# Kernel optimization log

Hardware: AMD Instinct MI355X
Metric: run time of the kernel (lower is better)

## Reference

```python
import jax
import jax.numpy as jnp
from jax import lax
import numpy as np

BETA = 0.5
IPOT_ITERS = 50
IPOT_K = 1
EPS = 1e-5  # F.normalize eps


def _l2_normalize(x, eps=EPS):
    n = jnp.linalg.norm(x, axis=-1, keepdims=True)
    return x / jnp.maximum(n, eps)


def cost_matrix_cosine(x, y):
    # x: [b, m, d], y: [b, n, d] -> 1 - cosine_sim : [b, m, n]
    return 1.0 - jnp.einsum('bmd,bnd->bmn', _l2_normalize(x), _l2_normalize(y))


def ipot(C, x_len, x_pad, y_len, y_pad, joint_pad, beta, iteration, k):
    # C: [b, m, n] (txt x img). Mirrors UNITER's ipot (no_grad).
    b, m, n = C.shape
    jp_T = jnp.swapaxes(joint_pad, 1, 2)                      # [b, n, m]
    A = jnp.where(jp_T, 0.0, jnp.exp(-jnp.swapaxes(C, 1, 2) / beta))  # [b, n, m]
    T0 = jnp.where(jp_T, 0.0, jnp.ones((b, n, m), C.dtype))
    sigma0 = jnp.where(x_pad, 0.0, 1.0 / x_len[:, None])      # [b, m]
    xl = x_len[:, None, None]
    yl = y_len[:, None, None]
    x_mask = (x_pad.astype(C.dtype) * 1e4)[:, None, :]        # [b, 1, m]
    y_mask = (y_pad.astype(C.dtype) * 1e4)[:, None, :]        # [b, 1, n]

    def outer(carry, _):
        T, sigma = carry
        Q = A * T                                             # [b, n, m]
        def inner(sig, _):
            # sig: [b, m]
            qs = jnp.einsum('bnm,bm->bn', Q, sig)[:, None, :]  # [b, 1, n]
            delta = 1.0 / (yl * qs + y_mask)                   # [b, 1, n]
            sig_new = 1.0 / (xl * jnp.matmul(delta, Q) + x_mask)  # [b, 1, m]
            return sig_new[:, 0, :], delta
        sigma, deltas = lax.scan(inner, sigma, None, length=k)
        delta = deltas[-1]                                     # [b, 1, n]
        T = delta[:, 0, :, None] * Q * sigma[:, None, :]       # [b, n, m]
        return (T, sigma), None

    (T, _), _ = lax.scan(outer, (T0, sigma0), None, length=iteration)
    return jnp.where(jp_T, 0.0, T)


def optimal_transport_dist(txt_emb, img_emb, txt_pad, img_pad,
                           beta=BETA, iteration=IPOT_ITERS, k=IPOT_K):
    cost = cost_matrix_cosine(txt_emb, img_emb)               # [b, tl, il]
    joint_pad = txt_pad[:, :, None] | img_pad[:, None, :]
    cost = jnp.where(joint_pad, 0.0, cost)
    txt_len = (txt_pad.shape[1] - jnp.sum(txt_pad, axis=1)).astype(cost.dtype)
    img_len = (img_pad.shape[1] - jnp.sum(img_pad, axis=1)).astype(cost.dtype)
    T = ipot(lax.stop_gradient(cost), txt_len, txt_pad, img_len, img_pad,
             joint_pad, beta, iteration, k)                   # [b, il, tl]
    T = lax.stop_gradient(T)
    # trace(cost @ T) without materializing [b, tl, tl]
    return jnp.einsum('bmn,bnm->b', cost, T)


def setup_inputs() -> dict:
    key = jax.random.key(0)
    ks = jax.random.split(key, 6)
    B, TL, IL, D = 256, 128, 100, 768
    sequence_output = jax.random.normal(ks[0], (B, TL + IL, D), dtype=jnp.float32)
    input_ids = jax.random.randint(ks[1], (B, TL), 0, 30522)
    image_feat = jax.random.normal(ks[2], (B, IL, D), dtype=jnp.float32)
    # realistic padding: valid prefix of random length, padded suffix
    txt_len = jax.random.randint(ks[3], (B,), TL // 2, TL + 1)
    img_len = jax.random.randint(ks[4], (B,), IL // 2, IL + 1)
    txt_pad = jnp.arange(TL)[None, :] >= txt_len[:, None]
    img_pad = jnp.arange(IL)[None, :] >= img_len[:, None]
    is_correct = jax.random.randint(ks[5], (B,), 0, 2)
    return {
        'sequence_output': sequence_output,
        'input_ids': input_ids,
        'image_feat': image_feat,
        'txt_pad': txt_pad,
        'img_pad': img_pad,
        'is_correct': is_correct,
    }


def reference(sequence_output, input_ids, image_feat, txt_pad, img_pad, is_correct):
    tl = input_ids.shape[1]
    il = image_feat.shape[1]
    txt_emb = sequence_output[:, :tl, :].astype(jnp.float32)
    img_emb = sequence_output[:, tl:tl + il, :].astype(jnp.float32)
    ot_dist = optimal_transport_dist(txt_emb, img_emb, txt_pad, img_pad)
    ot_dist = ot_dist.astype(sequence_output.dtype)
    pos = is_correct == 1
    neg = is_correct == 0
    pos_sum = jnp.sum(jnp.where(pos, ot_dist, 0.0))
    neg_sum = jnp.sum(jnp.where(neg, ot_dist, 0.0))
    denom = jnp.sum(pos) + jnp.sum(neg)
    ot_loss = (pos_sum - neg_sum) / denom.astype(ot_dist.dtype)
    return ot_loss


if __name__ == '__main__':
    out = reference(**setup_inputs())
    print(out)
```

## Files before the change

### kernel.cpp

```cpp
#include <hip/hip_runtime.h>
#include <math.h>
#include <stdint.h>

#define TL 128
#define IL 100
#define NP 112
#define DIM 768
#define NSEQ 228
#define KT 32
#define NT 512
#define NWAVE 8
#define ITERS 50
#define XROW 72

typedef float f32x4 __attribute__((ext_vector_type(4)));
typedef short short8 __attribute__((ext_vector_type(8)));

__device__ __forceinline__ uint16_t f2bf(float x) {
    union { float f; uint32_t u; } v; v.f = x;
    uint32_t r = v.u + 0x7FFFu + ((v.u >> 16) & 1u);
    return (uint16_t)(r >> 16);
}
__device__ __forceinline__ float bf2f(uint16_t h) {
    union { float f; uint32_t u; } v; v.u = ((uint32_t)h) << 16;
    return v.f;
}

__device__ __forceinline__ float xorsum32(float x) {
    x += __shfl_xor(x, 1);
    x += __shfl_xor(x, 2);
    x += __shfl_xor(x, 4);
    x += __shfl_xor(x, 8);
    x += __shfl_xor(x, 16);
    return x;
}

__global__ void __launch_bounds__(NT, 2)
WRA_ot_kernel(const float* __restrict__ seq,
              const int* __restrict__ txt_pad,
              const int* __restrict__ img_pad,
              const int* __restrict__ is_correct,
              float* __restrict__ out, int nblocks)
{
    __shared__ __align__(16) union {
        struct {
            uint16_t X[TL * XROW];
            uint16_t Y[NP * XROW];
        } g;
        float As[448 * 32];
        float wp[2][7][TL];
    } u;
    __shared__ __align__(16) float sums[NSEQ];
    __shared__ __align__(16) float xm[TL];
    __shared__ __align__(16) float ym[NP];
    __shared__ __align__(16) float inx[TL];
    __shared__ __align__(16) float iny[NP];
    __shared__ float red[NWAVE];
    __shared__ int cnt[2];

    const int t    = threadIdx.x;
    const int b    = blockIdx.x;
    const int w    = t >> 6;
    const int lane = t & 63;

    if (t < 2) cnt[t] = 0;
    if (t < NSEQ) sums[t] = 0.0f;
    __syncthreads();
    if (t < TL) {
        int p = txt_pad[b * TL + t] ? 1 : 0;
        xm[t] = p ? 1e4f : 0.0f;
        if (p) atomicAdd(&cnt[0], 1);
    } else if (t < TL + IL) {
        int p = img_pad[b * IL + (t - TL)] ? 1 : 0;
        ym[t - TL] = p ? 1e4f : 0.0f;
        if (p) atomicAdd(&cnt[1], 1);
    } else if (t < TL + NP) {
        ym[t - TL] = 1e4f;
    }

    const float* Xg = seq + (size_t)b * NSEQ * DIM;
    const float* Yg = Xg + (size_t)TL * DIM;

    const float* gp[4];
    uint16_t*    dp[4];
    int   srow[4];
    bool  act[4];
    float nrm[4];
    float4 v[4];
#pragma unroll
    for (int r = 0; r < 4; r++) {
        int f = t + NT * r;
        act[r] = (f < 1824);
        nrm[r] = 0.0f;
        int f2 = act[r] ? f : 0;
        bool isX = (f2 < 1024);
        int row = isX ? (f2 >> 3) : ((f2 - 1024) >> 3);
        int kc  = (f2 & 7) << 2;
        gp[r] = (isX ? Xg : Yg) + row * DIM + kc;
        int nq  = ((kc >> 3) + row) & 3;
        dp[r] = (isX ? u.g.X : u.g.Y) + row * XROW + nq * 8 + (kc & 7);
        srow[r] = isX ? row : (TL + row);
    }
    {
        uint32_t* y32 = (uint32_t*)u.g.Y;
        for (int i = IL * (XROW/2) + t; i < NP * (XROW/2); i += NT) y32[i] = 0;
    }
#pragma unroll
    for (int r = 0; r < 4; r++) if (act[r]) v[r] = *(const float4*)(gp[r]);

    const int wm = w >> 1;
    const int wn = w & 1;
    const int NQ = wn ? 3 : 4;
    f32x4 acc[2][4];
#pragma unroll
    for (int a = 0; a < 2; a++)
#pragma unroll
        for (int q = 0; q < 4; q++) acc[a][q] = (f32x4){0.f, 0.f, 0.f, 0.f};

    const int lr = lane & 15, lq = lane >> 4;
    for (int c = 0; c < 24; c++) {
        __syncthreads();
#pragma unroll
        for (int r = 0; r < 4; r++) if (act[r]) {
            float4 x = v[r];
            nrm[r] += x.x*x.x + x.y*x.y + x.z*x.z + x.w*x.w;
            uint16_t h0 = f2bf(x.x), h1 = f2bf(x.y), h2 = f2bf(x.z), h3 = f2bf(x.w);
            uint16_t l0 = f2bf(x.x - bf2f(h0)), l1 = f2bf(x.y - bf2f(h1));
            uint16_t l2 = f2bf(x.z - bf2f(h2)), l3 = f2bf(x.w - bf2f(h3));
            uint64_t hq  = (uint64_t)h0 | ((uint64_t)h1<<16) | ((uint64_t)h2<<32) | ((uint64_t)h3<<48);
            uint64_t lq8 = (uint64_t)l0 | ((uint64_t)l1<<16) | ((uint64_t)l2<<32) | ((uint64_t)l3<<48);
            *(uint64_t*)(dp[r])      = hq;
            *(uint64_t*)(dp[r] + 32) = lq8;
            if (c < 23) v[r] = *(const float4*)(gp[r] + (c + 1) * KT);
        }
        __syncthreads();
        short8 ah[2], al[2], bh[4], bl[4];
#pragma unroll
        for (int a = 0; a < 2; a++) {
            int m = 16 * (2*wm + a) + lr;
            int base = m * XROW + 8 * ((lq + m) & 3);
            ah[a] = *(const short8*)&u.g.X[base];
            al[a] = *(const short8*)&u.g.X[base + 32];
        }
#pragma unroll
        for (int q = 0; q < 4; q++) if (q < NQ) {
            int n = 16 * (4*wn + q) + lr;
            int base = n * XROW + 8 * ((lq + n) & 3);
            bh[q] = *(const short8*)&u.g.Y[base];
            bl[q] = *(const short8*)&u.g.Y[base + 32];
        }
#pragma unroll
        for (int a = 0; a < 2; a++)
#pragma unroll
            for (int q = 0; q < 4; q++) if (q < NQ) {
                acc[a][q] = __builtin_amdgcn_mfma_f32_16x16x32_bf16(ah[a], bh[q], acc[a][q], 0, 0, 0);
                acc[a][q] = __builtin_amdgcn_mfma_f32_16x16x32_bf16(ah[a], bl[q], acc[a][q], 0, 0, 0);
                acc[a][q] = __builtin_amdgcn_mfma_f32_16x16x32_bf16(al[a], bh[q], acc[a][q], 0, 0, 0);
            }
    }

    __syncthreads();
#pragma unroll
    for (int r = 0; r < 4; r++) if (act[r]) atomicAdd(&sums[srow[r]], nrm[r]);
#pragma unroll
    for (int a = 0; a < 2; a++)
#pragma unroll
        for (int q = 0; q < 4; q++) if (q < NQ)
#pragma unroll
            for (int rg = 0; rg < 4; rg++) {
                int m = 16 * (2*wm + a) + 4*lq + rg;
                int n = 16 * (4*wn + q) + lr;
                int tp = (m >> 2) + ((n >> 3) << 5);
                int cell = (((n & 7) ^ (tp & 7)) << 2) + (m & 3);
                u.As[(tp << 5) + cell] = acc[a][q][rg];
            }
    __syncthreads();
    if (t < TL)            inx[t]      = 1.0f / fmaxf(sqrtf(sums[t]), 1e-5f);
    else if (t < NSEQ)     iny[t - TL] = 1.0f / fmaxf(sqrtf(sums[t]), 1e-5f);
    else if (t < TL + NP)  iny[t - TL] = 1.0f;
    __syncthreads();

    const float xlen = (float)(TL - cnt[0]);
    const float ylen = (float)(IL - cnt[1]);
    const int mI = lane & 31;
    const int nI = t >> 5;
    const bool activeN = (nI < 14);

    float rx[4], xmv[4], ry[8], ymv[8];
    {
        float4 a0 = *(const float4*)&inx[4*mI];
        rx[0]=a0.x; rx[1]=a0.y; rx[2]=a0.z; rx[3]=a0.w;
        float4 b0 = *(const float4*)&xm[4*mI];
        xmv[0]=b0.x; xmv[1]=b0.y; xmv[2]=b0.z; xmv[3]=b0.w;
        if (activeN) {
            float4 c0 = *(const float4*)&iny[8*nI], c1 = *(const float4*)&iny[8*nI + 4];
            ry[0]=c0.x; ry[1]=c0.y; ry[2]=c0.z; ry[3]=c0.w;
            ry[4]=c1.x; ry[5]=c1.y; ry[6]=c1.z; ry[7]=c1.w;
            float4 d0 = *(const float4*)&ym[8*nI], d1 = *(const float4*)&ym[8*nI + 4];
            ymv[0]=d0.x; ymv[1]=d0.y; ymv[2]=d0.z; ymv[3]=d0.w;
            ymv[4]=d1.x; ymv[5]=d1.y; ymv[6]=d1.z; ymv[7]=d1.w;
        } else {
#pragma unroll
            for (int j = 0; j < 8; j++) { ry[j] = 1.0f; ymv[j] = 1e4f; }
        }
    }

    float aa[8][4], qq[8][4];
    if (activeN) {
#pragma unroll
        for (int j = 0; j < 8; j++) {
            float4 d0 = *(const float4*)&u.As[(t << 5) + ((j ^ (t & 7)) << 2)];
            float dv[4] = {d0.x, d0.y, d0.z, d0.w};
#pragma unroll
            for (int i = 0; i < 4; i++) {
                bool pad = (xmv[i] > 0.0f) || (ymv[j] > 0.0f);
                float cc = pad ? 0.0f : (1.0f - dv[i] * rx[i] * ry[j]);
                float av = pad ? 0.0f : expf(-2.0f * cc);
                aa[j][i] = av; qq[j][i] = av;
            }
        }
    } else {
#pragma unroll
        for (int j = 0; j < 8; j++)
#pragma unroll
            for (int i = 0; i < 4; i++) { aa[j][i] = 0.0f; qq[j][i] = 0.0f; }
    }
    __syncthreads();

    float sg[4];
#pragma unroll
    for (int i = 0; i < 4; i++) sg[i] = (xmv[i] > 0.0f) ? 0.0f : (1.0f / xlen);

    float dl[8];
    for (int it = 0; it < ITERS; ++it) {
#pragma unroll
        for (int j = 0; j < 8; j++) {
            float pj = qq[j][0]*sg[0] + qq[j][1]*sg[1] + qq[j][2]*sg[2] + qq[j][3]*sg[3];
            pj = xorsum32(pj);
            dl[j] = __builtin_amdgcn_rcpf(ylen * pj + ymv[j]);
        }
        float sp[4];
#pragma unroll
        for (int i = 0; i < 4; i++) {
            float s = dl[0]*qq[0][i] + dl[1]*qq[1][i] + dl[2]*qq[2][i] + dl[3]*qq[3][i]
                    + dl[4]*qq[4][i] + dl[5]*qq[5][i] + dl[6]*qq[6][i] + dl[7]*qq[7][i];
            sp[i] = s + __shfl_xor(s, 32);
        }
        if (w < 7 && lane < 32) {
            *(float4*)&u.wp[it & 1][w][4 * mI] = make_float4(sp[0], sp[1], sp[2], sp[3]);
        }
        __syncthreads();
        {
            float4 s0 = *(const float4*)&u.wp[it & 1][0][4*mI];
            float4 s1 = *(const float4*)&u.wp[it & 1][1][4*mI];
            float4 s2 = *(const float4*)&u.wp[it & 1][2][4*mI];
            float4 s3 = *(const float4*)&u.wp[it & 1][3][4*mI];
            float4 s4 = *(const float4*)&u.wp[it & 1][4][4*mI];
            float4 s5 = *(const float4*)&u.wp[it & 1][5][4*mI];
            float4 s6 = *(const float4*)&u.wp[it & 1][6][4*mI];
            float t0 = s0.x+s1.x+s2.x+s3.x+s4.x+s5.x+s6.x;
            float t1 = s0.y+s1.y+s2.y+s3.y+s4.y+s5.y+s6.y;
            float t2 = s0.z+s1.z+s2.z+s3.z+s4.z+s5.z+s6.z;
            float t3 = s0.w+s1.w+s2.w+s3.w+s4.w+s5.w+s6.w;
            sg[0] = __builtin_amdgcn_rcpf(xlen*t0 + xmv[0]);
            sg[1] = __builtin_amdgcn_rcpf(xlen*t1 + xmv[1]);
            sg[2] = __builtin_amdgcn_rcpf(xlen*t2 + xmv[2]);
            sg[3] = __builtin_amdgcn_rcpf(xlen*t3 + xmv[3]);
        }
        if (it < ITERS - 1) {
#pragma unroll
            for (int j = 0; j < 8; j++) {
                float dj = dl[j];
#pragma unroll
                for (int i = 0; i < 4; i++)
                    qq[j][i] = (qq[j][i] * aa[j][i]) * (dj * sg[i]);
            }
        }
    }

    float local = 0.0f;
#pragma unroll
    for (int j = 0; j < 8; j++)
#pragma unroll
        for (int i = 0; i < 4; i++) {
            float av = aa[j][i];
            float cc = (av > 0.0f) ? (-0.5f * logf(av)) : 0.0f;
            local += cc * qq[j][i] * (dl[j] * sg[i]);
        }
    local = xorsum32(local);
    local += __shfl_xor(local, 32);
    if (lane == 0) red[w] = local;
    __syncthreads();
    if (t == 0) {
        float tot = red[0] + red[1] + red[2] + red[3] + red[4] + red[5] + red[6] + red[7];
        float sgn = (is_correct[b] == 1) ? 1.0f : -1.0f;
        atomicAdd(out, sgn * tot / (float)nblocks);
    }
}

extern "C" void kernel_launch(void* const* d_in, const int* in_sizes, int n_in,
                              void* d_out, int out_size, void* d_ws, size_t ws_size,
                              hipStream_t stream) {
    const float* seq   = (const float*)d_in[0];
    const int* txt_pad = (const int*)d_in[3];
    const int* img_pad = (const int*)d_in[4];
    const int* is_corr = (const int*)d_in[5];
    float* out = (float*)d_out;
    const int B = in_sizes[5];

    hipMemsetAsync(out, 0, sizeof(float), stream);
    WRA_ot_kernel<<<B, NT, 0, stream>>>(seq, txt_pad, img_pad, is_corr, out, B);
}
```

Measured before the change: 377.0 us.

## Double-buffer GEMM staging with two-deep register prefetch and one barrier per step

Replaces the single LDS staging area for the bf16 hi/lo split of the cosine GEMM with two buffers. Global float4 loads are now prefetched two chunks ahead in two register sets, so conversion and store of chunk c+1 overlap the MFMA work on chunk c. This cuts the loop to one barrier per step instead of two. It also uses a new XOR-swizzled 64-element row layout and a custom barrier that waits only on LDS counters. The cost is more registers and LDS, which may reduce occupancy under the two-blocks-per-CU launch bound.

Result: slower. 438.3 us (+16.3%).

```diff
diff --git a/kernel.cpp b/kernel.cpp
--- a/kernel.cpp
+++ b/kernel.cpp
@@ -11,7 +11,6 @@
 #define NT 512
 #define NWAVE 8
 #define ITERS 50
-#define XROW 72
 
 typedef float f32x4 __attribute__((ext_vector_type(4)));
 typedef short short8 __attribute__((ext_vector_type(8)));
@@ -33,6 +32,13 @@
     x += __shfl_xor(x, 8);
     x += __shfl_xor(x, 16);
     return x;
+}
+
+__device__ __forceinline__ void gemm_barrier() {
+    __builtin_amdgcn_sched_barrier(0);
+    asm volatile("s_waitcnt lgkmcnt(0)" ::: "memory");
+    __builtin_amdgcn_s_barrier();
+    __builtin_amdgcn_sched_barrier(0);
 }
 
 __global__ void __launch_bounds__(NT, 2)
@@ -43,10 +49,7 @@
               float* __restrict__ out, int nblocks)
 {
     __shared__ __align__(16) union {
-        struct {
-            uint16_t X[TL * XROW];
-            uint16_t Y[NP * XROW];
-        } g;
+        uint16_t stg[2][240 * 64];
         float As[448 * 32];
         float wp[2][7][TL];
     } u;
@@ -82,11 +85,10 @@
     const float* Yg = Xg + (size_t)TL * DIM;
 
     const float* gp[4];
-    uint16_t*    dp[4];
+    int   off_hi[4];
     int   srow[4];
     bool  act[4];
     float nrm[4];
-    float4 v[4];
 #pragma unroll
     for (int r = 0; r < 4; r++) {
         int f = t + NT * r;
@@ -97,16 +99,21 @@
         int row = isX ? (f2 >> 3) : ((f2 - 1024) >> 3);
         int kc  = (f2 & 7) << 2;
         gp[r] = (isX ? Xg : Yg) + row * DIM + kc;
-        int nq  = ((kc >> 3) + row) & 3;
-        dp[r] = (isX ? u.g.X : u.g.Y) + row * XROW + nq * 8 + (kc & 7);
-        srow[r] = isX ? row : (TL + row);
+        int rr = isX ? row : (TL + row);
+        srow[r] = rr;
+        int q = (f2 & 7) >> 1;
+        int h = f2 & 1;
+        int s = (q + rr + (rr >> 3)) & 7;
+        off_hi[r] = rr * 64 + 8 * s + 4 * h;
     }
     {
-        uint32_t* y32 = (uint32_t*)u.g.Y;
-        for (int i = IL * (XROW/2) + t; i < NP * (XROW/2); i += NT) y32[i] = 0;
-    }
-#pragma unroll
-    for (int r = 0; r < 4; r++) if (act[r]) v[r] = *(const float4*)(gp[r]);
+        uint32_t* s32 = (uint32_t*)&u.stg[0][0];
+        for (int i = t; i < 384 * 2; i += NT) {
+            int par = (i < 384) ? 0 : 1;
+            int off = i - par * 384;
+            s32[par * 7680 + 228 * 32 + off] = 0;
+        }
+    }
 
     const int wm = w >> 1;
     const int wn = w & 1;
@@ -118,36 +125,62 @@
         for (int q = 0; q < 4; q++) acc[a][q] = (f32x4){0.f, 0.f, 0.f, 0.f};
 
     const int lr = lane & 15, lq = lane >> 4;
-    for (int c = 0; c < 24; c++) {
-        __syncthreads();
+
+    auto convert_store = [&](const float4* vv, int par) {
+        uint16_t* base = &u.stg[par][0];
 #pragma unroll
         for (int r = 0; r < 4; r++) if (act[r]) {
-            float4 x = v[r];
+            float4 x = vv[r];
             nrm[r] += x.x*x.x + x.y*x.y + x.z*x.z + x.w*x.w;
             uint16_t h0 = f2bf(x.x), h1 = f2bf(x.y), h2 = f2bf(x.z), h3 = f2bf(x.w);
             uint16_t l0 = f2bf(x.x - bf2f(h0)), l1 = f2bf(x.y - bf2f(h1));
             uint16_t l2 = f2bf(x.z - bf2f(h2)), l3 = f2bf(x.w - bf2f(h3));
             uint64_t hq  = (uint64_t)h0 | ((uint64_t)h1<<16) | ((uint64_t)h2<<32) | ((uint64_t)h3<<48);
             uint64_t lq8 = (uint64_t)l0 | ((uint64_t)l1<<16) | ((uint64_t)l2<<32) | ((uint64_t)l3<<48);
-            *(uint64_t*)(dp[r])      = hq;
-            *(uint64_t*)(dp[r] + 32) = lq8;
-            if (c < 23) v[r] = *(const float4*)(gp[r] + (c + 1) * KT);
-        }
-        __syncthreads();
+            *(uint64_t*)(base + off_hi[r])        = hq;
+            *(uint64_t*)(base + (off_hi[r] ^ 32)) = lq8;
+        }
+    };
+
+    float4 va[4], vb[4];
+#pragma unroll
+    for (int r = 0; r < 4; r++) if (act[r]) va[r] = *(const float4*)(gp[r]);
+#pragma unroll
+    for (int r = 0; r < 4; r++) if (act[r]) vb[r] = *(const float4*)(gp[r] + KT);
+    convert_store(va, 0);
+#pragma unroll
+    for (int r = 0; r < 4; r++) if (act[r]) va[r] = *(const float4*)(gp[r] + 2 * KT);
+    gemm_barrier();
+
+    for (int c = 0; c < 24; c++) {
+        const int p = c & 1;
+        if (c < 23) {
+            convert_store((c & 1) ? va : vb, p ^ 1);
+            if (c < 21) {
+                float4* vv = (c & 1) ? va : vb;
+#pragma unroll
+                for (int r = 0; r < 4; r++) if (act[r])
+                    vv[r] = *(const float4*)(gp[r] + (c + 3) * KT);
+            }
+        }
+        const uint16_t* base = &u.stg[p][0];
         short8 ah[2], al[2], bh[4], bl[4];
 #pragma unroll
         for (int a = 0; a < 2; a++) {
             int m = 16 * (2*wm + a) + lr;
-            int base = m * XROW + 8 * ((lq + m) & 3);
-            ah[a] = *(const short8*)&u.g.X[base];
-            al[a] = *(const short8*)&u.g.X[base + 32];
+            int s = (lq + m + (m >> 3)) & 7;
+            int ao = m * 64 + 8 * s;
+            ah[a] = *(const short8*)(base + ao);
+            al[a] = *(const short8*)(base + (ao ^ 32));
         }
 #pragma unroll
         for (int q = 0; q < 4; q++) if (q < NQ) {
-            int n = 16 * (4*wn + q) + lr;
-            int base = n * XROW + 8 * ((lq + n) & 3);
-            bh[q] = *(const short8*)&u.g.Y[base];
-            bl[q] = *(const short8*)&u.g.Y[base + 32];
+            int n  = 16 * (4*wn + q) + lr;
+            int rr = TL + n;
+            int s  = (lq + rr + (rr >> 3)) & 7;
+            int bo = rr * 64 + 8 * s;
+            bh[q] = *(const short8*)(base + bo);
+            bl[q] = *(const short8*)(base + (bo ^ 32));
         }
 #pragma unroll
         for (int a = 0; a < 2; a++)
@@ -157,9 +190,9 @@
                 acc[a][q] = __builtin_amdgcn_mfma_f32_16x16x32_bf16(ah[a], bl[q], acc[a][q], 0, 0, 0);
                 acc[a][q] = __builtin_amdgcn_mfma_f32_16x16x32_bf16(al[a], bh[q], acc[a][q], 0, 0, 0);
             }
-    }
-
-    __syncthreads();
+        gemm_barrier();
+    }
+
 #pragma unroll
     for (int r = 0; r < 4; r++) if (act[r]) atomicAdd(&sums[srow[r]], nrm[r]);
 #pragma unroll
```
